# Performance work log

Measured on AMD Instinct MI355X. Metric: run time of the kernel, lower is better.

## Reference

```python
import jax, jax.numpy as jnp
import numpy as np

N = 100000          # num nodes
E = 1600000         # num edges
C = 64              # num_classes
F_DIM = 512         # feature_dim
FH = 32             # feature_hidden_dim
DH = 16             # degree_hidden_dim
MAXDEG = 128        # degree-embedding table size (degrees clipped)
K = 2               # expert_select (top-k)


def setup_inputs() -> dict:
    key = jax.random.key(0)
    ks = jax.random.split(key, 24)
    def g(i, shape, scale=0.05):
        return jax.random.normal(ks[i], shape, dtype=jnp.float32) * scale
    inp = {
        'logits': jax.random.normal(ks[0], (N, C), dtype=jnp.float32),
        'features': jax.random.normal(ks[1], (N, F_DIM), dtype=jnp.float32),
        'edge_index': jax.random.randint(ks[2], (2, E), 0, N, dtype=jnp.int64),
        # expert 0: [logits, features] -> in = C + FH = 96
        'Wf0': g(3, (F_DIM, FH)), 'bf0': jnp.zeros((FH,), jnp.float32),
        'W0': g(4, (C + FH, C)), 'b0': jnp.zeros((C,), jnp.float32),
        # expert 1: [logits, degrees] -> in = C + DH = 80
        'Emb1': g(5, (MAXDEG, DH)),
        'W1': g(6, (C + DH, C)), 'b1': jnp.zeros((C,), jnp.float32),
        # expert 2: [features, degrees] -> in = FH + DH = 48
        'Wf2': g(7, (F_DIM, FH)), 'bf2': jnp.zeros((FH,), jnp.float32),
        'Emb2': g(8, (MAXDEG, DH)),
        'W2': g(9, (FH + DH, C)), 'b2': jnp.zeros((C,), jnp.float32),
        # gating: concat [logits, proj(features), deg_emb] -> C+FH+DH = 112
        'Wfg': g(10, (F_DIM, FH)), 'bfg': jnp.zeros((FH,), jnp.float32),
        'Embg': g(11, (MAXDEG, DH)),
        'w_gate': g(12, (C + FH + DH, 3)),
    }
    return inp


def _gcn_conv(x, W, b, src, dst, n):
    # PyG GCNConv with self-loops: D^-1/2 (A+I) D^-1/2 (x W) + b
    h = x @ W                                            # [N, out]
    deg = jnp.zeros((n,), x.dtype).at[dst].add(1.0) + 1.0
    dinv = jax.lax.rsqrt(deg)
    coef = dinv[src] * dinv[dst]                          # per-edge norm
    agg = jnp.zeros_like(h).at[dst].add(h[src] * coef[:, None])
    return agg + h * (dinv * dinv)[:, None] + b


def reference(logits, features, edge_index, Wf0, bf0, W0, b0, Emb1, W1, b1,
              Wf2, bf2, Emb2, W2, b2, Wfg, bfg, Embg, w_gate):
    src, dst = edge_index[0], edge_index[1]
    n = logits.shape[0]
    # on-the-fly degree: degree(row) + degree(col), clipped to table size
    deg_i = (jnp.zeros((n,), jnp.int32).at[src].add(1)
             .at[dst].add(1))
    deg_idx = jnp.clip(deg_i, 0, MAXDEG - 1)

    # --- experts (GCN backbone, num_layers=2 -> single conv to C) ---
    x0 = jnp.concatenate([logits, features @ Wf0 + bf0], axis=-1)
    y0 = _gcn_conv(x0, W0, b0, src, dst, n)
    x1 = jnp.concatenate([logits, Emb1[deg_idx]], axis=-1)
    y1 = _gcn_conv(x1, W1, b1, src, dst, n)
    x2 = jnp.concatenate([features @ Wf2 + bf2, Emb2[deg_idx]], axis=-1)
    y2 = _gcn_conv(x2, W2, b2, src, dst, n)

    # --- gating (clean top-k, noisy gating disabled in eval) ---
    gate_in = jnp.concatenate([logits, features @ Wfg + bfg, Embg[deg_idx]], axis=-1)
    clean = gate_in @ w_gate                              # [N, num_experts]
    top_vals, top_idx = jax.lax.top_k(clean, K)           # [N, K]
    gk = jax.nn.softmax(top_vals, axis=1)                 # renormalized top-k
    gates = jnp.zeros_like(clean).at[jnp.arange(n)[:, None], top_idx].add(gk)

    experts = jnp.stack([y0, y1, y2], axis=1)             # [N, num_experts, C]
    combined = jnp.einsum('ne,nec->nc', gates, experts)   # [N, C]

    # node-wise temperature scaling of base-model logits
    temperature = jax.nn.softplus(combined)
    return logits * temperature
```

## Files before the change

### kernel.cpp

```cpp
#include <hip/hip_runtime.h>
#include <hip/hip_bf16.h>
#include <math.h>


#define XD 160
#define CC 64
#define BCAP 16384

typedef __attribute__((ext_vector_type(8))) short short8;
typedef __attribute__((ext_vector_type(4))) float f32x4;

static __device__ inline unsigned pk_bf16(float a, float b) {
  __hip_bfloat162 h;
  h.x = __float2bfloat16(a);
  h.y = __float2bfloat16(b);
  return *reinterpret_cast<unsigned*>(&h);
}
static __device__ inline unsigned short bf16u(float f) {
  __hip_bfloat16 h = __float2bfloat16(f);
  return *reinterpret_cast<unsigned short*>(&h);
}
static __device__ inline float bf_lo(unsigned u) {
  unsigned v = u << 16;
  return __builtin_bit_cast(float, v);
}
static __device__ inline float bf_hi(unsigned u) {
  unsigned v = u & 0xffff0000u;
  return __builtin_bit_cast(float, v);
}

__global__ void k_init(unsigned* __restrict__ cursorS, unsigned* __restrict__ cursorE,
                       int nbk) {
  int b = blockIdx.x * blockDim.x + threadIdx.x;
  if (b < nbk) {
    cursorS[b] = (unsigned)b * BCAP;
    cursorE[b] = (unsigned)b * BCAP;
  }
}

__global__ __launch_bounds__(256) void k_fused(
    const int* __restrict__ ei, int E, int nbk,
    unsigned* __restrict__ cursorS, int* __restrict__ partIds,
    unsigned* __restrict__ cursorE, int2* __restrict__ partE,
    const float* __restrict__ feat, const unsigned short* __restrict__ Wb,
    const float* __restrict__ bf0, const float* __restrict__ bf2,
    const float* __restrict__ Wv4, const float* __restrict__ logits,
    unsigned* __restrict__ Xu, float* __restrict__ CFG,
    int nblk_part, int nblk_proj, int n) {
  __shared__ int h[256];
  __shared__ unsigned baseb[256];

  int g = blockIdx.x / 6;
  int r = blockIdx.x % 6;

  if (r == 0) {
    if (g >= nblk_part) return;
    int t = threadIdx.x;
    for (int i = t; i < nbk; i += 256) h[i] = 0;
    __syncthreads();
    int base = g * 4096;
    int myv[16], mybk[16];
#pragma unroll
    for (int q = 0; q < 16; ++q) {
      int idx = base + q * 256 + t;
      if (idx < E) {
        int v = ei[idx];
        myv[q] = v; mybk[q] = v >> 9;
        atomicAdd(&h[mybk[q]], 1);
      } else mybk[q] = -1;
    }
    __syncthreads();
    for (int i = t; i < nbk; i += 256)
      baseb[i] = h[i] ? atomicAdd(&cursorS[i], (unsigned)h[i]) : 0u;
    __syncthreads();
    for (int i = t; i < nbk; i += 256) h[i] = 0;
    __syncthreads();
#pragma unroll
    for (int q = 0; q < 16; ++q) {
      int bk = mybk[q];
      if (bk >= 0) {
        int rr = atomicAdd(&h[bk], 1);
        unsigned pos = baseb[bk] + rr;
        if (pos < (unsigned)(bk + 1) * BCAP) partIds[pos] = myv[q];
      }
    }
    return;
  }

  if (r == 1) {
    if (g >= nblk_part) return;
    int t = threadIdx.x;
    for (int i = t; i < nbk; i += 256) h[i] = 0;
    __syncthreads();
    int base = g * 4096;
    int myd[16], mys[16];
#pragma unroll
    for (int q = 0; q < 16; ++q) {
      int e = base + q * 256 + t;
      if (e < E) {
        mys[q] = ei[e];
        myd[q] = ei[E + e];
        atomicAdd(&h[myd[q] >> 9], 1);
      } else myd[q] = -1;
    }
    __syncthreads();
    for (int i = t; i < nbk; i += 256)
      baseb[i] = h[i] ? atomicAdd(&cursorE[i], (unsigned)h[i]) : 0u;
    __syncthreads();
    for (int i = t; i < nbk; i += 256) h[i] = 0;
    __syncthreads();
#pragma unroll
    for (int q = 0; q < 16; ++q) {
      if (myd[q] >= 0) {
        int bk = myd[q] >> 9;
        int rr = atomicAdd(&h[bk], 1);
        unsigned pos = baseb[bk] + rr;
        if (pos < (unsigned)(bk + 1) * BCAP) {
          int2 v; v.x = myd[q]; v.y = mys[q];
          partE[pos] = v;
        }
      }
    }
    return;
  }

  int p = g * 4 + (r - 2);
  if (p >= nblk_proj) return;
  int l = threadIdx.x & 63;
  int gw = p * 4 + (threadIdx.x >> 6);
  int node_in = gw * 16 + (l & 15);
  int nc = node_in < n ? node_in : n - 1;
  const float* frow = feat + (size_t)nc * 512 + ((l >> 4) << 3);

  f32x4 acc[4];
#pragma unroll
  for (int q = 0; q < 4; ++q) acc[q] = (f32x4){0.f, 0.f, 0.f, 0.f};
  float cfg0 = 0.f, cfg1 = 0.f, cfg2 = 0.f;

  for (int ks = 0; ks < 16; ++ks) {
    float4 fa = *(const float4*)&frow[ks * 32];
    float4 fb = *(const float4*)&frow[ks * 32 + 4];
    float fv[8] = {fa.x, fa.y, fa.z, fa.w, fb.x, fb.y, fb.z, fb.w};
    const float* wvp = Wv4 + (ks * 32 + ((l >> 4) << 3)) * 4;
#pragma unroll
    for (int j = 0; j < 8; ++j) {
      float4 v = *(const float4*)&wvp[j * 4];
      cfg0 += fv[j] * v.x;
      cfg1 += fv[j] * v.y;
      cfg2 += fv[j] * v.z;
    }
    unsigned short pa[8];
#pragma unroll
    for (int j = 0; j < 8; ++j) pa[j] = bf16u(fv[j]);
    short8 af = *(const short8*)pa;
#pragma unroll
    for (int nt = 0; nt < 4; ++nt) {
      short8 bfv = *(const short8*)&Wb[(size_t)((ks * 4 + nt) * 64 + l) * 8];
      acc[nt] = __builtin_amdgcn_mfma_f32_16x16x32_bf16(af, bfv, acc[nt], 0, 0, 0);
    }
  }

  cfg0 += __shfl_xor(cfg0, 16); cfg0 += __shfl_xor(cfg0, 32);
  cfg1 += __shfl_xor(cfg1, 16); cfg1 += __shfl_xor(cfg1, 32);
  cfg2 += __shfl_xor(cfg2, 16); cfg2 += __shfl_xor(cfg2, 32);
  if (l < 16 && node_in < n) {
    float4 cc = *(const float4*)&Wv4[512 * 4];
    CFG[node_in] = cfg0 + cc.x;
    CFG[n + node_in] = cfg1 + cc.y;
    CFG[2 * (size_t)n + node_in] = cfg2 + cc.z;
  }

  unsigned short* Xus = (unsigned short*)Xu;
#pragma unroll
  for (int nt = 0; nt < 4; ++nt) {
    int col = (nt << 4) + (l & 15);
    float bias = (col < 32) ? bf0[col] : bf2[col - 32];
    int fidx = 64 + col;
#pragma unroll
    for (int rr = 0; rr < 4; ++rr) {
      int nd = gw * 16 + ((l >> 4) << 2) + rr;
      if (nd < n) Xus[(size_t)nd * 128 + fidx] = bf16u(acc[nt][rr] + bias);
    }
  }

  int nb16 = gw * 16;
#pragma unroll
  for (int q = 0; q < 8; ++q) {
    int ii = q * 64 + l;
    int nd = nb16 + (ii >> 5);
    int pp = ii & 31;
    if (nd < n) {
      float2 lg = *(const float2*)&logits[(size_t)nd * 64 + 2 * pp];
      Xu[(size_t)nd * 64 + pp] = pk_bf16(lg.x, lg.y);
    }
  }
}

__global__ __launch_bounds__(256) void k_h3(const int* __restrict__ partIds,
                                            const unsigned* __restrict__ cursorS,
                                            const int2* __restrict__ partE,
                                            const unsigned* __restrict__ cursorE,
                                            int nbk, int n,
                                            int* __restrict__ indeg, int* __restrict__ outdeg) {
  __shared__ int cnt[512];
  int b = blockIdx.x;
  int t = threadIdx.x;
  for (int i = t; i < 512; i += 256) cnt[i] = 0;
  __syncthreads();
  if (b < nbk) {
    unsigned s = (unsigned)b * BCAP, e = cursorS[b];
    for (unsigned i = s + t; i < e; i += 256) {
      int v = partIds[i];
      atomicAdd(&cnt[v & 511], 1);
    }
    __syncthreads();
    for (int i = t; i < 512; i += 256) {
      int node = b * 512 + i;
      if (node < n) outdeg[node] = cnt[i];
    }
  } else {
    int bb = b - nbk;
    unsigned s = (unsigned)bb * BCAP, e = cursorE[bb];
    for (unsigned i = s + t; i < e; i += 256) {
      int d = partE[i].x;
      atomicAdd(&cnt[d & 511], 1);
    }
    __syncthreads();
    for (int i = t; i < 512; i += 256) {
      int node = bb * 512 + i;
      if (node < n) indeg[node] = cnt[i];
    }
  }
}

__global__ void k_scan1(const int* __restrict__ indeg, int n, int* __restrict__ bsum) {
  __shared__ int red[1024];
  int tid = threadIdx.x;
  int i = blockIdx.x * 1024 + tid;
  red[tid] = (i < n) ? indeg[i] : 0;
  __syncthreads();
  for (int s = 512; s > 0; s >>= 1) {
    if (tid < s) red[tid] += red[tid + s];
    __syncthreads();
  }
  if (tid == 0) bsum[blockIdx.x] = red[0];
}

__global__ void k_scan2(int* __restrict__ bsum, int nb, int* __restrict__ row_start, int n) {
  if (threadIdx.x == 0 && blockIdx.x == 0) {
    int run = 0;
    for (int b = 0; b < nb; ++b) { int t = bsum[b]; bsum[b] = run; run += t; }
    row_start[n] = run;
  }
}

__global__ void k_scan3(const int* __restrict__ indeg, const int* __restrict__ outdeg,
                        int n, const int* __restrict__ bsum,
                        int* __restrict__ row_start, float* __restrict__ dinv,
                        int* __restrict__ deg_i) {
  __shared__ int sc[1024];
  int tid = threadIdx.x;
  int i = blockIdx.x * 1024 + tid;
  int ind = (i < n) ? indeg[i] : 0;
  sc[tid] = ind;
  __syncthreads();
  for (int ofs = 1; ofs < 1024; ofs <<= 1) {
    int t = (tid >= ofs) ? sc[tid - ofs] : 0;
    __syncthreads();
    sc[tid] += t;
    __syncthreads();
  }
  if (i < n) {
    int incl = sc[tid];
    row_start[i] = incl - ind + bsum[blockIdx.x];
    dinv[i] = rsqrtf((float)ind + 1.0f);
    deg_i[i] = ind + outdeg[i];
  }
}

__global__ __launch_bounds__(256) void k_fill2(const int2* __restrict__ partE,
                                               const unsigned* __restrict__ cursorE,
                                               const int* __restrict__ row_start,
                                               const float* __restrict__ dinv,
                                               const int* __restrict__ deg_i,
                                               int2* __restrict__ ec) {
  __shared__ int cur[512];
  int b = blockIdx.x;
  int t = threadIdx.x;
  for (int i = t; i < 512; i += 256) cur[i] = 0;
  __syncthreads();
  unsigned s0 = (unsigned)b * BCAP, e0 = cursorE[b];
  for (unsigned i = s0 + t; i < e0; i += 256) {
    int2 rec = partE[i];
    int d = rec.x, s = rec.y;
    int r = atomicAdd(&cur[d & 511], 1);
    int pos = row_start[d] + r;
    int dg = deg_i[s]; if (dg > 127) dg = 127;
    int2 v;
    v.x = s | (dg << 20);
    v.y = __float_as_int(dinv[s] * dinv[d]);
    ec[pos] = v;
  }
}

__global__ void k_wv(const float* __restrict__ Wfg, const float* __restrict__ bfg,
                     const float* __restrict__ wg, float* __restrict__ Wv4) {
  int k = blockIdx.x * blockDim.x + threadIdx.x;
  if (k >= 512) return;
  float a0 = 0.f, a1 = 0.f, a2 = 0.f;
  for (int j = 0; j < 32; ++j) {
    float w = Wfg[k * 32 + j];
    a0 += w * wg[(64 + j) * 3 + 0];
    a1 += w * wg[(64 + j) * 3 + 1];
    a2 += w * wg[(64 + j) * 3 + 2];
  }
  float4 v; v.x = a0; v.y = a1; v.z = a2; v.w = 0.f;
  *(float4*)&Wv4[k * 4] = v;
  if (k == 0) {
    float c0 = 0.f, c1 = 0.f, c2 = 0.f;
    for (int j = 0; j < 32; ++j) {
      float b = bfg[j];
      c0 += b * wg[(64 + j) * 3 + 0];
      c1 += b * wg[(64 + j) * 3 + 1];
      c2 += b * wg[(64 + j) * 3 + 2];
    }
    float4 c; c.x = c0; c.y = c1; c.z = c2; c.w = 0.f;
    *(float4*)&Wv4[512 * 4] = c;
  }
}

__global__ void k_wb(const float* __restrict__ Wf0, const float* __restrict__ Wf2,
                     unsigned short* __restrict__ Wb) {
  int tid = blockIdx.x * blockDim.x + threadIdx.x;
  if (tid >= 16 * 4 * 64) return;
  int l = tid & 63;
  int nt = (tid >> 6) & 3;
  int ks = tid >> 8;
  int col = (nt << 4) + (l & 15);
  int rowb = ks * 32 + ((l >> 4) << 3);
  const float* wsrc = (col < 32) ? (Wf0 + col) : (Wf2 + (col - 32));
  unsigned short pb[8];
#pragma unroll
  for (int j = 0; j < 8; ++j)
    pb[j] = bf16u(wsrc[(size_t)(rowb + j) * 32]);
  *(uint4*)&Wb[(size_t)tid * 8] = *(const uint4*)pb;
}

__global__ void k_wc(const float* __restrict__ W0, const float* __restrict__ W1,
                     const float* __restrict__ W2, unsigned short* __restrict__ Wc) {
  int tid = blockIdx.x * blockDim.x + threadIdx.x;
  if (tid >= 7 * 4 * 64) return;
  int l = tid & 63;
  int nt = (tid >> 6) & 3;
  int st = tid >> 8;
  int col = (nt << 4) + (l & 15);
  int kb = st * 32 + ((l >> 4) << 3);
  unsigned short pb[8];
#pragma unroll
  for (int j = 0; j < 8; ++j) {
    int k = kb + j;
    float w;
    if (k < 96)       w = W0[(size_t)k * 64 + col];
    else if (k < 176) w = W1[(size_t)(k - 96) * 64 + col];
    else              w = W2[(size_t)(k - 176) * 64 + col];
    pb[j] = bf16u(w);
  }
  *(uint4*)&Wc[(size_t)tid * 8] = *(const uint4*)pb;
}

__global__ __launch_bounds__(256) void k_agg(
    const unsigned* __restrict__ Xu, unsigned* __restrict__ Ztn,
    const int* __restrict__ row_start, const int2* __restrict__ ec,
    const int* __restrict__ deg_i,
    const float* __restrict__ Emb1, const float* __restrict__ Emb2,
    const float* __restrict__ dinv, int n) {
  int w = threadIdx.x >> 6, l = threadIdx.x & 63;
  int node = blockIdx.x * 4 + w;
  if (node >= n) return;
  int beg = row_start[node], end = row_start[node + 1];

  const float* etab = (l < 8) ? (Emb1 + 2 * l) : (Emb2 + 2 * (l - 8));

  float ax = 0.f, ay = 0.f, bx = 0.f, by = 0.f;
  int i = beg;
  for (; i + 8 <= end; i += 8) {
    int2 e[8];
    unsigned u[8];
#pragma unroll
    for (int q = 0; q < 8; ++q) e[q] = ec[i + q];
#pragma unroll
    for (int q = 0; q < 8; ++q) u[q] = Xu[(size_t)(e[q].x & 0xFFFFF) * 64 + l];
#pragma unroll
    for (int q = 0; q < 8; ++q) {
      float c = __int_as_float(e[q].y);
      ax += c * bf_lo(u[q]);
      ay += c * bf_hi(u[q]);
    }
    if (l < 16) {
#pragma unroll
      for (int q = 0; q < 8; ++q) {
        float c = __int_as_float(e[q].y);
        float2 ev = *(const float2*)&etab[(e[q].x >> 20) * 16];
        bx += c * ev.x;
        by += c * ev.y;
      }
    }
  }
  for (; i + 4 <= end; i += 4) {
    int2 e[4];
    unsigned u[4];
#pragma unroll
    for (int q = 0; q < 4; ++q) e[q] = ec[i + q];
#pragma unroll
    for (int q = 0; q < 4; ++q) u[q] = Xu[(size_t)(e[q].x & 0xFFFFF) * 64 + l];
#pragma unroll
    for (int q = 0; q < 4; ++q) {
      float c = __int_as_float(e[q].y);
      ax += c * bf_lo(u[q]);
      ay += c * bf_hi(u[q]);
    }
    if (l < 16) {
#pragma unroll
      for (int q = 0; q < 4; ++q) {
        float c = __int_as_float(e[q].y);
        float2 ev = *(const float2*)&etab[(e[q].x >> 20) * 16];
        bx += c * ev.x;
        by += c * ev.y;
      }
    }
  }
  for (; i < end; ++i) {
    int2 e0 = ec[i];
    int s0 = e0.x & 0xFFFFF;
    float c0 = __int_as_float(e0.y);
    unsigned u0 = Xu[(size_t)s0 * 64 + l];
    ax += c0 * bf_lo(u0); ay += c0 * bf_hi(u0);
    if (l < 16) {
      float2 ev0 = *(const float2*)&etab[(e0.x >> 20) * 16];
      bx += c0 * ev0.x; by += c0 * ev0.y;
    }
  }
  float di = dinv[node];
  float c2s = di * di;
  {
    unsigned u = Xu[(size_t)node * 64 + l];
    ax += c2s * bf_lo(u);
    ay += c2s * bf_hi(u);
    if (l < 16) {
      int dg = deg_i[node]; if (dg > 127) dg = 127;
      float2 ev = *(const float2*)&etab[dg * 16];
      bx += c2s * ev.x;
      by += c2s * ev.y;
    }
  }
  Ztn[(size_t)node * 80 + l] = pk_bf16(ax, ay);
  if (l < 16)
    Ztn[(size_t)node * 80 + 64 + l] = pk_bf16(bx, by);
}

__global__ __launch_bounds__(256) void k_final2(
    const unsigned* __restrict__ Ztn, const float* __restrict__ logits,
    const float* __restrict__ CFG, const int* __restrict__ deg_i,
    const unsigned short* __restrict__ Wc,
    const float* __restrict__ b0, const float* __restrict__ b1,
    const float* __restrict__ b2,
    const float* __restrict__ Embg, const float* __restrict__ wg,
    float* __restrict__ out, int n) {
  int l = threadIdx.x & 63;
  int gw = blockIdx.x * 4 + (threadIdx.x >> 6);
  int node0 = gw * 16;

  float g0 = 0.f, g1 = 0.f, g2 = 0.f;
  if (l < 16) {
    int node = node0 + l;
    int nc = node < n ? node : n - 1;
    float c0 = 0.f, c1 = 0.f, c2 = 0.f;
    const float* lgr = logits + (size_t)nc * 64;
#pragma unroll
    for (int q = 0; q < 16; ++q) {
      float4 v = *(const float4*)&lgr[q * 4];
      const float* p = (const float*)&v;
#pragma unroll
      for (int j = 0; j < 4; ++j) {
        int k = q * 4 + j;
        c0 += p[j] * wg[k * 3 + 0];
        c1 += p[j] * wg[k * 3 + 1];
        c2 += p[j] * wg[k * 3 + 2];
      }
    }
    {
      int dg = deg_i[nc]; if (dg > 127) dg = 127;
      const float* egr = Embg + dg * 16;
#pragma unroll
      for (int q = 0; q < 4; ++q) {
        float4 v = *(const float4*)&egr[q * 4];
        const float* p = (const float*)&v;
#pragma unroll
        for (int j = 0; j < 4; ++j) {
          int k = 96 + q * 4 + j;
          c0 += p[j] * wg[k * 3 + 0];
          c1 += p[j] * wg[k * 3 + 1];
          c2 += p[j] * wg[k * 3 + 2];
        }
      }
    }
    c0 += CFG[nc];
    c1 += CFG[n + nc];
    c2 += CFG[2 * (size_t)n + nc];

    int i0 = 0; float t0 = c0;
    if (c1 > t0) { t0 = c1; i0 = 1; }
    if (c2 > t0) { t0 = c2; i0 = 2; }
    float t1 = -3.4e38f; int i1 = 0;
    if (i0 != 0) { t1 = c0; i1 = 0; }
    if (i0 != 1 && c1 > t1) { t1 = c1; i1 = 1; }
    if (i0 != 2 && c2 > t1) { t1 = c2; i1 = 2; }
    float e1v = expf(t1 - t0);
    float gsum = 1.0f + e1v;
    float gA = 1.0f / gsum, gB = e1v / gsum;
    g0 = (i0 == 0) ? gA : (i1 == 0) ? gB : 0.f;
    g1 = (i0 == 1) ? gA : (i1 == 1) ? gB : 0.f;
    g2 = (i0 == 2) ? gA : (i1 == 2) ? gB : 0.f;
  }

  float gA0 = __shfl(g0, l & 15);
  float gA1 = __shfl(g1, l & 15);
  float gA2 = __shfl(g2, l & 15);

  int nodeA = node0 + (l & 15);
  int ncA = nodeA < n ? nodeA : n - 1;
  const unsigned* zrow = Ztn + (size_t)ncA * 80;

  f32x4 acc[4];
#pragma unroll
  for (int q = 0; q < 4; ++q) acc[q] = (f32x4){0.f, 0.f, 0.f, 0.f};

#pragma unroll
  for (int st = 0; st < 7; ++st) {
    int k0 = st * 32 + ((l >> 4) << 3);
    int ub = (k0 < 96)  ? (k0 >> 1)
           : (k0 < 160) ? ((k0 - 96) >> 1)
           : (k0 < 176) ? (64 + ((k0 - 160) >> 1))
           : (k0 < 208) ? (48 + ((k0 - 176) >> 1))
                        : (72 + ((k0 - 208) >> 1));
    float ge = (k0 < 96) ? gA0 : (k0 < 176) ? gA1 : gA2;
    uint4 zu = *(const uint4*)&zrow[ub];
    unsigned zz[4] = {zu.x, zu.y, zu.z, zu.w};
    unsigned short pa[8];
#pragma unroll
    for (int q2 = 0; q2 < 4; ++q2) {
      pa[2 * q2]     = bf16u(ge * bf_lo(zz[q2]));
      pa[2 * q2 + 1] = bf16u(ge * bf_hi(zz[q2]));
    }
    short8 af = *(const short8*)pa;
#pragma unroll
    for (int nt = 0; nt < 4; ++nt) {
      short8 bfv = *(const short8*)&Wc[(size_t)((st * 4 + nt) * 64 + l) * 8];
      acc[nt] = __builtin_amdgcn_mfma_f32_16x16x32_bf16(af, bfv, acc[nt], 0, 0, 0);
    }
  }

#pragma unroll
  for (int nt = 0; nt < 4; ++nt) {
    int col = (nt << 4) + (l & 15);
    float bb0 = b0[col], bb1 = b1[col], bb2 = b2[col];
#pragma unroll
    for (int r = 0; r < 4; ++r) {
      int rid = ((l >> 4) << 2) + r;
      float gg0 = __shfl(g0, rid);
      float gg1 = __shfl(g1, rid);
      float gg2 = __shfl(g2, rid);
      int node = node0 + rid;
      if (node < n) {
        float v = acc[nt][r] + gg0 * bb0 + gg1 * bb1 + gg2 * bb2;
        float sp = fmaxf(v, 0.f) + log1pf(expf(-fabsf(v)));
        float lg = logits[(size_t)node * 64 + col];
        out[(size_t)node * 64 + col] = lg * sp;
      }
    }
  }
}

extern "C" void kernel_launch(void* const* d_in, const int* in_sizes, int n_in,
                              void* d_out, int out_size, void* d_ws, size_t ws_size,
                              hipStream_t stream) {
  const float* logits = (const float*)d_in[0];
  const float* feat   = (const float*)d_in[1];
  const int*   ei     = (const int*)d_in[2];
  const float* Wf0 = (const float*)d_in[3];
  const float* bf0 = (const float*)d_in[4];
  const float* W0  = (const float*)d_in[5];
  const float* b0  = (const float*)d_in[6];
  const float* Emb1= (const float*)d_in[7];
  const float* W1  = (const float*)d_in[8];
  const float* b1  = (const float*)d_in[9];
  const float* Wf2 = (const float*)d_in[10];
  const float* bf2 = (const float*)d_in[11];
  const float* Emb2= (const float*)d_in[12];
  const float* W2  = (const float*)d_in[13];
  const float* b2  = (const float*)d_in[14];
  const float* Wfg = (const float*)d_in[15];
  const float* bfg = (const float*)d_in[16];
  const float* Embg= (const float*)d_in[17];
  const float* wg  = (const float*)d_in[18];

  int n = in_sizes[0] / 64;
  int E = in_sizes[2] / 2;
  int nbk = (n + 511) / 512;
  int nb2 = 2 * nbk;

  char* base = (char*)d_ws;
  size_t off = 0;
  auto alloc = [&](size_t bytes) -> void* {
    void* p = base + off;
    off += bytes;
    off = (off + 255) & ~(size_t)255;
    return p;
  };
  unsigned* cursorS = (unsigned*)alloc((size_t)nbk * 4);
  unsigned* cursorE = (unsigned*)alloc((size_t)nbk * 4);
  int*   partIds   = (int*)alloc((size_t)nbk * BCAP * 4);
  int2*  partE     = (int2*)alloc((size_t)nbk * BCAP * 8);
  int*   indeg     = (int*)alloc((size_t)n * 4);
  int*   outdeg    = (int*)alloc((size_t)n * 4);
  int*   deg_i     = (int*)alloc((size_t)n * 4);
  int*   row_start = (int*)alloc(((size_t)n + 1) * 4);
  int*   bsum      = (int*)alloc(1024 * 4);
  float* dinv      = (float*)alloc((size_t)n * 4);
  int2*  ec        = (int2*)alloc((size_t)E * 8);
  float* CFG       = (float*)alloc((size_t)n * 3 * 4);
  float* Wv4       = (float*)alloc((size_t)513 * 4 * 4);
  unsigned short* Wb = (unsigned short*)alloc((size_t)16 * 4 * 64 * 8 * 2);
  unsigned short* Wc = (unsigned short*)alloc((size_t)7 * 4 * 64 * 8 * 2);
  unsigned* Xu     = (unsigned*)alloc((size_t)n * 64 * 4);
  unsigned* Ztn    = (unsigned*)alloc((size_t)n * 80 * 4);
  (void)ws_size;

  int nb_scan = (n + 1023) / 1024;
  int nblk_part = (E + 4095) / 4096;
  int nw16 = (n + 15) / 16;
  int nblk_proj = (nw16 + 3) / 4;
  int G = nblk_part;
  int gp = (nblk_proj + 3) / 4;
  if (gp > G) G = gp;

  k_init<<<(nbk + 255) / 256, 256, 0, stream>>>(cursorS, cursorE, nbk);
  k_wv<<<2, 256, 0, stream>>>(Wfg, bfg, wg, Wv4);
  k_wb<<<16, 256, 0, stream>>>(Wf0, Wf2, Wb);
  k_wc<<<7, 256, 0, stream>>>(W0, W1, W2, Wc);
  k_fused<<<G * 6, 256, 0, stream>>>(ei, E, nbk,
                                     cursorS, partIds, cursorE, partE,
                                     feat, Wb, bf0, bf2, Wv4, logits, Xu, CFG,
                                     nblk_part, nblk_proj, n);
  k_h3<<<nb2, 256, 0, stream>>>(partIds, cursorS, partE, cursorE,
                                nbk, n, indeg, outdeg);
  k_scan1<<<nb_scan, 1024, 0, stream>>>(indeg, n, bsum);
  k_scan2<<<1, 64, 0, stream>>>(bsum, nb_scan, row_start, n);
  k_scan3<<<nb_scan, 1024, 0, stream>>>(indeg, outdeg, n, bsum, row_start, dinv, deg_i);
  k_fill2<<<nbk, 256, 0, stream>>>(partE, cursorE, row_start, dinv, deg_i, ec);
  k_agg<<<(n + 3) / 4, 256, 0, stream>>>(Xu, Ztn, row_start, ec, deg_i, Emb1, Emb2, dinv, n);
  k_final2<<<(nw16 + 3) / 4, 256, 0, stream>>>(Ztn, logits, CFG, deg_i, Wc, b0, b1, b2,
                                               Embg, wg, (float*)d_out, n);
}
```

Before: 336.7 us.

## Fuse neighbor aggregation with final expert MFMA and gating kernel

Merges the aggregation kernel and the final combine kernel into one. Each block aggregates 16 nodes, four per wave, into a shared-memory tile, then each wave computes one 16-column MFMA tile of the combined expert output. This removes the global round trip of the Ztn intermediate and one kernel launch. In exchange there is a block-wide barrier, per-wave serial work over four nodes, and the gating prologue is now computed redundantly by all four waves.

```diff
diff --git a/kernel.cpp b/kernel.cpp
--- a/kernel.cpp
+++ b/kernel.cpp
@@ -368,107 +368,105 @@
   *(uint4*)&Wc[(size_t)tid * 8] = *(const uint4*)pb;
 }
 
-__global__ __launch_bounds__(256) void k_agg(
-    const unsigned* __restrict__ Xu, unsigned* __restrict__ Ztn,
-    const int* __restrict__ row_start, const int2* __restrict__ ec,
-    const int* __restrict__ deg_i,
+__global__ __launch_bounds__(256) void k_aggfin(
+    const unsigned* __restrict__ Xu, const int* __restrict__ row_start,
+    const int2* __restrict__ ec, const int* __restrict__ deg_i,
     const float* __restrict__ Emb1, const float* __restrict__ Emb2,
-    const float* __restrict__ dinv, int n) {
-  int w = threadIdx.x >> 6, l = threadIdx.x & 63;
-  int node = blockIdx.x * 4 + w;
-  if (node >= n) return;
-  int beg = row_start[node], end = row_start[node + 1];
-
-  const float* etab = (l < 8) ? (Emb1 + 2 * l) : (Emb2 + 2 * (l - 8));
-
-  float ax = 0.f, ay = 0.f, bx = 0.f, by = 0.f;
-  int i = beg;
-  for (; i + 8 <= end; i += 8) {
-    int2 e[8];
-    unsigned u[8];
-#pragma unroll
-    for (int q = 0; q < 8; ++q) e[q] = ec[i + q];
-#pragma unroll
-    for (int q = 0; q < 8; ++q) u[q] = Xu[(size_t)(e[q].x & 0xFFFFF) * 64 + l];
-#pragma unroll
-    for (int q = 0; q < 8; ++q) {
-      float c = __int_as_float(e[q].y);
-      ax += c * bf_lo(u[q]);
-      ay += c * bf_hi(u[q]);
-    }
-    if (l < 16) {
-#pragma unroll
-      for (int q = 0; q < 8; ++q) {
-        float c = __int_as_float(e[q].y);
-        float2 ev = *(const float2*)&etab[(e[q].x >> 20) * 16];
-        bx += c * ev.x;
-        by += c * ev.y;
-      }
-    }
-  }
-  for (; i + 4 <= end; i += 4) {
-    int2 e[4];
-    unsigned u[4];
-#pragma unroll
-    for (int q = 0; q < 4; ++q) e[q] = ec[i + q];
-#pragma unroll
-    for (int q = 0; q < 4; ++q) u[q] = Xu[(size_t)(e[q].x & 0xFFFFF) * 64 + l];
-#pragma unroll
-    for (int q = 0; q < 4; ++q) {
-      float c = __int_as_float(e[q].y);
-      ax += c * bf_lo(u[q]);
-      ay += c * bf_hi(u[q]);
-    }
-    if (l < 16) {
-#pragma unroll
-      for (int q = 0; q < 4; ++q) {
-        float c = __int_as_float(e[q].y);
-        float2 ev = *(const float2*)&etab[(e[q].x >> 20) * 16];
-        bx += c * ev.x;
-        by += c * ev.y;
-      }
-    }
-  }
-  for (; i < end; ++i) {
-    int2 e0 = ec[i];
-    int s0 = e0.x & 0xFFFFF;
-    float c0 = __int_as_float(e0.y);
-    unsigned u0 = Xu[(size_t)s0 * 64 + l];
-    ax += c0 * bf_lo(u0); ay += c0 * bf_hi(u0);
-    if (l < 16) {
-      float2 ev0 = *(const float2*)&etab[(e0.x >> 20) * 16];
-      bx += c0 * ev0.x; by += c0 * ev0.y;
-    }
-  }
-  float di = dinv[node];
-  float c2s = di * di;
-  {
-    unsigned u = Xu[(size_t)node * 64 + l];
-    ax += c2s * bf_lo(u);
-    ay += c2s * bf_hi(u);
-    if (l < 16) {
-      int dg = deg_i[node]; if (dg > 127) dg = 127;
-      float2 ev = *(const float2*)&etab[dg * 16];
-      bx += c2s * ev.x;
-      by += c2s * ev.y;
-    }
-  }
-  Ztn[(size_t)node * 80 + l] = pk_bf16(ax, ay);
-  if (l < 16)
-    Ztn[(size_t)node * 80 + 64 + l] = pk_bf16(bx, by);
-}
-
-__global__ __launch_bounds__(256) void k_final2(
-    const unsigned* __restrict__ Ztn, const float* __restrict__ logits,
-    const float* __restrict__ CFG, const int* __restrict__ deg_i,
+    const float* __restrict__ dinv,
+    const float* __restrict__ logits, const float* __restrict__ CFG,
     const unsigned short* __restrict__ Wc,
     const float* __restrict__ b0, const float* __restrict__ b1,
     const float* __restrict__ b2,
     const float* __restrict__ Embg, const float* __restrict__ wg,
     float* __restrict__ out, int n) {
+  __shared__ unsigned zl[16][80];
+
   int l = threadIdx.x & 63;
-  int gw = blockIdx.x * 4 + (threadIdx.x >> 6);
-  int node0 = gw * 16;
+  int w = threadIdx.x >> 6;
+  int node0 = blockIdx.x * 16;
+
+  const float* etab = (l < 8) ? (Emb1 + 2 * l) : (Emb2 + 2 * (l - 8));
+  for (int j = 0; j < 4; ++j) {
+    int node = node0 + w * 4 + j;
+    if (node >= n) break;
+    int beg = row_start[node], end = row_start[node + 1];
+    float ax = 0.f, ay = 0.f, bx = 0.f, by = 0.f;
+    int i = beg;
+    for (; i + 8 <= end; i += 8) {
+      int2 e[8];
+      unsigned u[8];
+#pragma unroll
+      for (int q = 0; q < 8; ++q) e[q] = ec[i + q];
+#pragma unroll
+      for (int q = 0; q < 8; ++q) u[q] = Xu[(size_t)(e[q].x & 0xFFFFF) * 64 + l];
+#pragma unroll
+      for (int q = 0; q < 8; ++q) {
+        float c = __int_as_float(e[q].y);
+        ax += c * bf_lo(u[q]);
+        ay += c * bf_hi(u[q]);
+      }
+      if (l < 16) {
+#pragma unroll
+        for (int q = 0; q < 8; ++q) {
+          float c = __int_as_float(e[q].y);
+          float2 ev = *(const float2*)&etab[(e[q].x >> 20) * 16];
+          bx += c * ev.x;
+          by += c * ev.y;
+        }
+      }
+    }
+    for (; i + 4 <= end; i += 4) {
+      int2 e[4];
+      unsigned u[4];
+#pragma unroll
+      for (int q = 0; q < 4; ++q) e[q] = ec[i + q];
+#pragma unroll
+      for (int q = 0; q < 4; ++q) u[q] = Xu[(size_t)(e[q].x & 0xFFFFF) * 64 + l];
+#pragma unroll
+      for (int q = 0; q < 4; ++q) {
+        float c = __int_as_float(e[q].y);
+        ax += c * bf_lo(u[q]);
+        ay += c * bf_hi(u[q]);
+      }
+      if (l < 16) {
+#pragma unroll
+        for (int q = 0; q < 4; ++q) {
+          float c = __int_as_float(e[q].y);
+          float2 ev = *(const float2*)&etab[(e[q].x >> 20) * 16];
+          bx += c * ev.x;
+          by += c * ev.y;
+        }
+      }
+    }
+    for (; i < end; ++i) {
+      int2 e0 = ec[i];
+      int s0 = e0.x & 0xFFFFF;
+      float c0 = __int_as_float(e0.y);
+      unsigned u0 = Xu[(size_t)s0 * 64 + l];
+      ax += c0 * bf_lo(u0); ay += c0 * bf_hi(u0);
+      if (l < 16) {
+        float2 ev0 = *(const float2*)&etab[(e0.x >> 20) * 16];
+        bx += c0 * ev0.x; by += c0 * ev0.y;
+      }
+    }
+    float di = dinv[node];
+    float c2s = di * di;
+    {
+      unsigned u = Xu[(size_t)node * 64 + l];
+      ax += c2s * bf_lo(u);
+      ay += c2s * bf_hi(u);
+      if (l < 16) {
+        int dg = deg_i[node]; if (dg > 127) dg = 127;
+        float2 ev = *(const float2*)&etab[dg * 16];
+        bx += c2s * ev.x;
+        by += c2s * ev.y;
+      }
+    }
+    int lr = w * 4 + j;
+    zl[lr][l] = pk_bf16(ax, ay);
+    if (l < 16) zl[lr][64 + l] = pk_bf16(bx, by);
+  }
+  __syncthreads();
 
   float g0 = 0.f, g1 = 0.f, g2 = 0.f;
   if (l < 16) {
@@ -527,13 +525,10 @@
   float gA1 = __shfl(g1, l & 15);
   float gA2 = __shfl(g2, l & 15);
 
-  int nodeA = node0 + (l & 15);
-  int ncA = nodeA < n ? nodeA : n - 1;
-  const unsigned* zrow = Ztn + (size_t)ncA * 80;
-
-  f32x4 acc[4];
-#pragma unroll
-  for (int q = 0; q < 4; ++q) acc[q] = (f32x4){0.f, 0.f, 0.f, 0.f};
+  const unsigned* zrow = &zl[l & 15][0];
+
+  f32x4 acc = (f32x4){0.f, 0.f, 0.f, 0.f};
+  int nt = w;
 
 #pragma unroll
   for (int st = 0; st < 7; ++st) {
@@ -553,15 +548,11 @@
       pa[2 * q2 + 1] = bf16u(ge * bf_hi(zz[q2]));
     }
     short8 af = *(const short8*)pa;
-#pragma unroll
-    for (int nt = 0; nt < 4; ++nt) {
-      short8 bfv = *(const short8*)&Wc[(size_t)((st * 4 + nt) * 64 + l) * 8];
-      acc[nt] = __builtin_amdgcn_mfma_f32_16x16x32_bf16(af, bfv, acc[nt], 0, 0, 0);
-    }
-  }
-
-#pragma unroll
-  for (int nt = 0; nt < 4; ++nt) {
+    short8 bfv = *(const short8*)&Wc[(size_t)((st * 4 + nt) * 64 + l) * 8];
+    acc = __builtin_amdgcn_mfma_f32_16x16x32_bf16(af, bfv, acc, 0, 0, 0);
+  }
+
+  {
     int col = (nt << 4) + (l & 15);
     float bb0 = b0[col], bb1 = b1[col], bb2 = b2[col];
 #pragma unroll
@@ -572,7 +563,7 @@
       float gg2 = __shfl(g2, rid);
       int node = node0 + rid;
       if (node < n) {
-        float v = acc[nt][r] + gg0 * bb0 + gg1 * bb1 + gg2 * bb2;
+        float v = acc[r] + gg0 * bb0 + gg1 * bb1 + gg2 * bb2;
         float sp = fmaxf(v, 0.f) + log1pf(expf(-fabsf(v)));
         float lg = logits[(size_t)node * 64 + col];
         out[(size_t)node * 64 + col] = lg * sp;
@@ -633,7 +624,6 @@
   unsigned short* Wb = (unsigned short*)alloc((size_t)16 * 4 * 64 * 8 * 2);
   unsigned short* Wc = (unsigned short*)alloc((size_t)7 * 4 * 64 * 8 * 2);
   unsigned* Xu     = (unsigned*)alloc((size_t)n * 64 * 4);
-  unsigned* Ztn    = (unsigned*)alloc((size_t)n * 80 * 4);
   (void)ws_size;
 
   int nb_scan = (n + 1023) / 1024;
@@ -658,7 +648,7 @@
   k_scan2<<<1, 64, 0, stream>>>(bsum, nb_scan, row_start, n);
   k_scan3<<<nb_scan, 1024, 0, stream>>>(indeg, outdeg, n, bsum, row_start, dinv, deg_i);
   k_fill2<<<nbk, 256, 0, stream>>>(partE, cursorE, row_start, dinv, deg_i, ec);
-  k_agg<<<(n + 3) / 4, 256, 0, stream>>>(Xu, Ztn, row_start, ec, deg_i, Emb1, Emb2, dinv, n);
-  k_final2<<<(nw16 + 3) / 4, 256, 0, stream>>>(Ztn, logits, CFG, deg_i, Wc, b0, b1, b2,
-                                               Embg, wg, (float*)d_out, n);
-}
+  k_aggfin<<<nw16, 256, 0, stream>>>(Xu, row_start, ec, deg_i, Emb1, Emb2, dinv,
+                                     logits, CFG, Wc, b0, b1, b2, Embg, wg,
+                                     (float*)d_out, n);
+}
```

New measurement: 333.3 us. Within noise of the previous version (-1.0%).
